# Kernel optimization log

Measured on AMD Instinct MI355X. Metric: run time of the kernel, lower is better.

## Reference

```python
import jax, jax.numpy as jnp
import numpy as np

N = 100000
E = 1_600_000
C_IN = 128
HID = 64
C_OUT = 64
HEADS = 3
NEG_SLOPE = 0.2  # PyG GATConv default leaky-relu slope


def setup_inputs() -> dict:
    key = jax.random.key(0)
    ks = jax.random.split(key, 8)
    return {
        "node_features": jax.random.normal(ks[0], (N, C_IN), jnp.float32),
        "edge_index": jax.random.randint(ks[1], (2, E), 0, N, jnp.int32),
        "edge_attributes": jax.random.uniform(ks[2], (E,), jnp.float32),
        "W1": jax.random.normal(ks[3], (C_IN, HID), jnp.float32) * 0.1,
        "b1": jnp.zeros((HID,), jnp.float32),
        "W2": jax.random.normal(ks[4], (HID, HEADS * C_OUT), jnp.float32) * 0.1,
        "b2": jnp.zeros((HEADS * C_OUT,), jnp.float32),
        "att_src": jax.random.normal(ks[5], (HEADS, C_OUT), jnp.float32) * 0.1,
        "att_dst": jax.random.normal(ks[6], (HEADS, C_OUT), jnp.float32) * 0.1,
    }


def reference(node_features, edge_index, edge_attributes, W1, b1, W2, b2, att_src, att_dst):
    n = node_features.shape[0]
    loops = jnp.arange(n, dtype=edge_index.dtype)
    # Both GCNConv and GATConv add self-loops by default (fill weight 1.0)
    src = jnp.concatenate([edge_index[0], loops])
    dst = jnp.concatenate([edge_index[1], loops])
    ew = jnp.concatenate([edge_attributes, jnp.ones((n,), node_features.dtype)])

    # ---- GCNConv: symmetric-normalized weighted scatter-add aggregation ----
    deg = jax.ops.segment_sum(ew, dst, num_segments=n)            # [N]
    dis = jnp.where(deg > 0, jax.lax.rsqrt(deg), 0.0)
    norm = dis[src] * ew * dis[dst]                               # [Et]
    xw = node_features @ W1                                       # [N, HID]
    x = jax.ops.segment_sum(xw[src] * norm[:, None], dst, num_segments=n) + b1
    x = jax.nn.relu(x)

    # ---- GATConv (heads concat): per-edge attention + segment softmax ----
    heads, c_out = att_src.shape
    g = (x @ W2).reshape(n, heads, c_out)                          # [N, H, F]
    a_src = jnp.sum(g * att_src, axis=-1)                          # [N, H]
    a_dst = jnp.sum(g * att_dst, axis=-1)                          # [N, H]
    alpha = jax.nn.leaky_relu(a_src[src] + a_dst[dst], NEG_SLOPE)  # [Et, H]
    amax = jax.ops.segment_max(alpha, dst, num_segments=n)         # softmax per dst node
    ex = jnp.exp(alpha - amax[dst])
    denom = jax.ops.segment_sum(ex, dst, num_segments=n)
    attn = ex / (denom[dst] + 1e-16)                               # [Et, H]
    out = jax.ops.segment_sum(g[src] * attn[:, :, None], dst, num_segments=n)
    out = out.reshape(n, heads * c_out) + b2                       # [N, H*F]

    # ---- global_mean_pool(x, None): mean over all nodes -> [1, H*F] ----
    return jnp.mean(out, axis=0, keepdims=True)
```

## Files before the change

### kernel.cpp

```cpp
#include <hip/hip_runtime.h>
#include <hip/hip_fp16.h>
#include <math.h>

typedef unsigned long long u64;
typedef unsigned int u32;

__device__ __forceinline__ float lrelu(float v) { return v > 0.f ? v : 0.2f * v; }

union H2U { __half2 h; u32 u; };


__global__ void k_hist(const int* __restrict__ dst, int* __restrict__ cnt, int E) {
    int e = blockIdx.x * 256 + threadIdx.x;
    if (e < E) atomicAdd(&cnt[dst[e]], 1);
}

__global__ __launch_bounds__(256) void k_scan1(const int* __restrict__ cnt,
                                               int* __restrict__ off,
                                               int* __restrict__ partials, int N) {
    __shared__ int sh[256];
    int tid = threadIdx.x;
    int base = blockIdx.x * 1024 + tid * 4;
    int v[4]; int tsum = 0;
#pragma unroll
    for (int i = 0; i < 4; i++) {
        int n = base + i;
        int c = (n < N) ? cnt[n] + 1 : 0;
        v[i] = tsum; tsum += c;
    }
    sh[tid] = tsum; __syncthreads();
    int mine = tsum;
    for (int o = 1; o < 256; o <<= 1) {
        int t = (tid >= o) ? sh[tid - o] : 0;
        __syncthreads();
        sh[tid] += t;
        __syncthreads();
    }
    int excl = sh[tid] - mine;
#pragma unroll
    for (int i = 0; i < 4; i++) {
        int n = base + i;
        if (n < N) off[n] = excl + v[i];
    }
    if (tid == 255) partials[blockIdx.x] = sh[255];
}

__global__ void k_scan2(int* __restrict__ partials, int nb) {
    __shared__ int sh[256];
    int tid = threadIdx.x;
    int v = (tid < nb) ? partials[tid] : 0;
    sh[tid] = v; __syncthreads();
    for (int o = 1; o < 256; o <<= 1) {
        int t = (tid >= o) ? sh[tid - o] : 0;
        __syncthreads();
        sh[tid] += t;
        __syncthreads();
    }
    if (tid < nb) partials[tid] = sh[tid] - v;
}

__global__ void k_scan3(int* __restrict__ off, int* __restrict__ cursor,
                        const int* __restrict__ partials, int N, int Et) {
    int base = blockIdx.x * 1024 + threadIdx.x * 4;
    int add = partials[blockIdx.x];
#pragma unroll
    for (int i = 0; i < 4; i++) {
        int n = base + i;
        if (n < N) { int o = off[n] + add; off[n] = o; cursor[n] = o; }
    }
    if (blockIdx.x == 0 && threadIdx.x == 0) { off[N] = Et; cursor[N] = Et; }
}

__global__ void k_fill(const int* __restrict__ src, const int* __restrict__ dst,
                       const float* __restrict__ ew, int* __restrict__ cursor,
                       u64* __restrict__ epk, int E, int Et) {
    int e = blockIdx.x * 256 + threadIdx.x;
    if (e >= Et) return;
    int s, d; float w;
    if (e < E) { s = src[e]; d = dst[e]; w = ew[e]; }
    else       { s = d = e - E; w = 1.0f; }
    int p = atomicAdd(&cursor[d], 1);
    epk[p] = ((u64)__float_as_uint(w) << 32) | (unsigned)s;
}

__global__ void k_degdis(const int* __restrict__ off, const u64* __restrict__ epk,
                         float* __restrict__ dis, int N) {
    int n = blockIdx.x * 256 + threadIdx.x;
    if (n >= N) return;
    int b = off[n], e2 = off[n + 1];
    float s = 0.f;
    for (int i = b; i < e2; i++) s += __uint_as_float((u32)(epk[i] >> 32));
    dis[n] = rsqrtf(s);
}


__global__ __launch_bounds__(256) void k_gemm1(const float* __restrict__ X,
                                               const float* __restrict__ W1,
                                               const float* __restrict__ dis,
                                               __half* __restrict__ xwh, int N) {
    __shared__ __align__(16) float Ws[128 * 64];
    __shared__ __align__(16) float Xs[32][129];
    int tid = threadIdx.x;
    int m0 = blockIdx.x * 32;
    const float4* W4 = (const float4*)W1;
    float4* Ws4 = (float4*)Ws;
#pragma unroll
    for (int i = 0; i < 8; i++) Ws4[tid + i * 256] = W4[tid + i * 256];
#pragma unroll
    for (int i = 0; i < 4; i++) {
        int idx = tid + i * 256;
        int r = idx >> 5;
        int c = idx & 31;
        float4 v = ((const float4*)(X + (size_t)(m0 + r) * 128))[c];
        Xs[r][c * 4 + 0] = v.x; Xs[r][c * 4 + 1] = v.y;
        Xs[r][c * 4 + 2] = v.z; Xs[r][c * 4 + 3] = v.w;
    }
    __syncthreads();
    int r = tid & 31;
    int c0 = (tid >> 5) * 8;
    float acc[8] = {0, 0, 0, 0, 0, 0, 0, 0};
#pragma unroll 4
    for (int k = 0; k < 128; k++) {
        float xv = Xs[r][k];
        const float4* wr = (const float4*)&Ws[k * 64 + c0];
        float4 w0 = wr[0], w1 = wr[1];
        acc[0] += xv * w0.x; acc[1] += xv * w0.y; acc[2] += xv * w0.z; acc[3] += xv * w0.w;
        acc[4] += xv * w1.x; acc[5] += xv * w1.y; acc[6] += xv * w1.z; acc[7] += xv * w1.w;
    }
    float dn = dis[m0 + r];
    H2U p0, p1, p2, p3;
    p0.h = __floats2half2_rn(acc[0] * dn, acc[1] * dn);
    p1.h = __floats2half2_rn(acc[2] * dn, acc[3] * dn);
    p2.h = __floats2half2_rn(acc[4] * dn, acc[5] * dn);
    p3.h = __floats2half2_rn(acc[6] * dn, acc[7] * dn);
    ((uint4*)(xwh + (size_t)(m0 + r) * 64))[c0 >> 3] = make_uint4(p0.u, p1.u, p2.u, p3.u);
}

__global__ __launch_bounds__(256) void k_gcn_agg(const int* __restrict__ off,
                                                 const u64* __restrict__ epk,
                                                 const float* __restrict__ dis,
                                                 const __half* __restrict__ xwh,
                                                 float* __restrict__ x, int N) {
    int lane = threadIdx.x & 63;
    int wv = threadIdx.x >> 6;
    int slot = lane >> 3;
    int f8 = lane & 7;
    int gw = blockIdx.x * 4 + wv;
    int stride = gridDim.x * 4;
    for (int n = gw; n < N; n += stride) {
        int b = off[n], en = off[n + 1];
        float acc[8] = {0, 0, 0, 0, 0, 0, 0, 0};
        for (int c = b; c < en; c += 64) {
            int idx = c + lane;
            int s = 0; float nw = 0.f;
            if (idx < en) {
                u64 pk = epk[idx];
                s = (int)(u32)pk;
                nw = __uint_as_float((u32)(pk >> 32));
            }
            int cc = min(64, en - c);
            for (int r = 0; r * 8 < cc; r++) {
                int eo = r * 8 + slot;
                int ss = __shfl(s, eo);
                float nn = __shfl(nw, eo);
                if (eo < cc) {
                    uint4 raw = ((const uint4*)(xwh + (size_t)ss * 64))[f8];
                    __half2* hp = (__half2*)&raw;
                    float2 q0 = __half22float2(hp[0]);
                    float2 q1 = __half22float2(hp[1]);
                    float2 q2 = __half22float2(hp[2]);
                    float2 q3 = __half22float2(hp[3]);
                    acc[0] += nn * q0.x; acc[1] += nn * q0.y;
                    acc[2] += nn * q1.x; acc[3] += nn * q1.y;
                    acc[4] += nn * q2.x; acc[5] += nn * q2.y;
                    acc[6] += nn * q3.x; acc[7] += nn * q3.y;
                }
            }
        }
#pragma unroll
        for (int j = 0; j < 8; j++) {
            acc[j] += __shfl_xor(acc[j], 8);
            acc[j] += __shfl_xor(acc[j], 16);
            acc[j] += __shfl_xor(acc[j], 32);
        }
        if (lane < 8) {
            float dn = dis[n];
            ((float4*)(x + (size_t)n * 64))[f8 * 2 + 0] =
                make_float4(acc[0] * dn, acc[1] * dn, acc[2] * dn, acc[3] * dn);
            ((float4*)(x + (size_t)n * 64))[f8 * 2 + 1] =
                make_float4(acc[4] * dn, acc[5] * dn, acc[6] * dn, acc[7] * dn);
        }
    }
}

__global__ __launch_bounds__(256) void k_gemm2(const float* __restrict__ x,
                                               const float* __restrict__ W2,
                                               const float* __restrict__ b1,
                                               __half* __restrict__ gh, int N) {
    __shared__ __align__(16) float Ws[64 * 192];
    __shared__ __align__(16) float Xs[32][65];
    __shared__ float b1s[64];
    int tid = threadIdx.x;
    int m0 = blockIdx.x * 32;
    if (tid < 64) b1s[tid] = b1[tid];
    __syncthreads();
    const float4* W4 = (const float4*)W2;
    float4* Ws4 = (float4*)Ws;
#pragma unroll
    for (int i = 0; i < 12; i++) Ws4[tid + i * 256] = W4[tid + i * 256];
#pragma unroll
    for (int i = 0; i < 2; i++) {
        int idx = tid + i * 256;
        int r = idx >> 4;
        int c4 = idx & 15;
        float4 v = ((const float4*)(x + (size_t)(m0 + r) * 64))[c4];
        v.x = fmaxf(v.x + b1s[c4 * 4 + 0], 0.f);
        v.y = fmaxf(v.y + b1s[c4 * 4 + 1], 0.f);
        v.z = fmaxf(v.z + b1s[c4 * 4 + 2], 0.f);
        v.w = fmaxf(v.w + b1s[c4 * 4 + 3], 0.f);
        Xs[r][c4 * 4 + 0] = v.x; Xs[r][c4 * 4 + 1] = v.y;
        Xs[r][c4 * 4 + 2] = v.z; Xs[r][c4 * 4 + 3] = v.w;
    }
    __syncthreads();
    int r = tid & 31;
    int c0 = (tid >> 5) * 24;
    float acc[24];
#pragma unroll
    for (int j = 0; j < 24; j++) acc[j] = 0.f;
#pragma unroll 4
    for (int k = 0; k < 64; k++) {
        float xv = Xs[r][k];
        const float4* wr = (const float4*)&Ws[k * 192 + c0];
#pragma unroll
        for (int q = 0; q < 6; q++) {
            float4 wv = wr[q];
            acc[q * 4 + 0] += xv * wv.x;
            acc[q * 4 + 1] += xv * wv.y;
            acc[q * 4 + 2] += xv * wv.z;
            acc[q * 4 + 3] += xv * wv.w;
        }
    }
    __half* outp = gh + (size_t)(m0 + r) * 192 + c0;
#pragma unroll
    for (int t = 0; t < 3; t++) {
        H2U p0, p1, p2, p3;
        p0.h = __floats2half2_rn(acc[t * 8 + 0], acc[t * 8 + 1]);
        p1.h = __floats2half2_rn(acc[t * 8 + 2], acc[t * 8 + 3]);
        p2.h = __floats2half2_rn(acc[t * 8 + 4], acc[t * 8 + 5]);
        p3.h = __floats2half2_rn(acc[t * 8 + 6], acc[t * 8 + 7]);
        ((uint4*)outp)[t] = make_uint4(p0.u, p1.u, p2.u, p3.u);
    }
}

__global__ __launch_bounds__(256) void k_att(const __half* __restrict__ gh,
                                             const float* __restrict__ att_src,
                                             const float* __restrict__ att_dst,
                                             float* __restrict__ asrc4,
                                             float* __restrict__ adst4, int N3) {
    __shared__ float as_s[192], ad_s[192];
    int tid = threadIdx.x;
    if (tid < 192) { as_s[tid] = att_src[tid]; ad_s[tid] = att_dst[tid]; }
    __syncthreads();
    int idx = blockIdx.x * 256 + tid;
    if (idx < N3) {
        int n = idx / 3, h = idx - 3 * n;
        const uint4* gp = (const uint4*)(gh + (size_t)n * 192 + h * 64);
        const float* av = as_s + h * 64;
        const float* bv = ad_s + h * 64;
        float sa = 0.f, sb = 0.f;
#pragma unroll
        for (int i = 0; i < 8; i++) {
            uint4 u = gp[i];
            __half2* hp = (__half2*)&u;
#pragma unroll
            for (int k = 0; k < 4; k++) {
                float2 f = __half22float2(hp[k]);
                int fi = i * 8 + k * 2;
                sa += f.x * av[fi] + f.y * av[fi + 1];
                sb += f.x * bv[fi] + f.y * bv[fi + 1];
            }
        }
        asrc4[(size_t)n * 4 + h] = sa;
        adst4[(size_t)n * 4 + h] = sb;
    }
}

__global__ __launch_bounds__(256) void k_gatsm(const int* __restrict__ off,
                                               const u64* __restrict__ epk,
                                               const float* __restrict__ asrc4,
                                               const float* __restrict__ adst4,
                                               u64* __restrict__ wpk, int N) {
    int n = blockIdx.x * 256 + threadIdx.x;
    if (n >= N) return;
    int b = off[n], en = off[n + 1];
    float4 ad = ((const float4*)adst4)[n];
    float m0 = -1e30f, m1 = -1e30f, m2 = -1e30f;
    for (int i = b; i < en; i++) {
        int s = (int)(u32)epk[i];
        float4 av = ((const float4*)asrc4)[s];
        m0 = fmaxf(m0, lrelu(av.x + ad.x));
        m1 = fmaxf(m1, lrelu(av.y + ad.y));
        m2 = fmaxf(m2, lrelu(av.z + ad.z));
    }
    float s0 = 0.f, s1 = 0.f, s2 = 0.f;
    for (int i = b; i < en; i++) {
        int s = (int)(u32)epk[i];
        float4 av = ((const float4*)asrc4)[s];
        s0 += __expf(lrelu(av.x + ad.x) - m0);
        s1 += __expf(lrelu(av.y + ad.y) - m1);
        s2 += __expf(lrelu(av.z + ad.z) - m2);
    }
    float i0 = 8192.f / s0, i1 = 8192.f / s1, i2 = 8192.f / s2;
    for (int i = b; i < en; i++) {
        int s = (int)(u32)epk[i];
        float4 av = ((const float4*)asrc4)[s];
        u32 q0 = __float2uint_rn(__expf(lrelu(av.x + ad.x) - m0) * i0);
        u32 q1 = __float2uint_rn(__expf(lrelu(av.y + ad.y) - m1) * i1);
        u32 q2 = __float2uint_rn(__expf(lrelu(av.z + ad.z) - m2) * i2);
        u64 pk = (u64)q0 | ((u64)q1 << 21) | ((u64)q2 << 42);
        atomicAdd(&wpk[s], pk);
    }
}

__global__ __launch_bounds__(192) void k_wsum(const u64* __restrict__ wpk,
                                              const __half* __restrict__ gh,
                                              float* __restrict__ gsum, int N) {
    int j = threadIdx.x;
    int sh = 21 * (j >> 6);
    int gs = gridDim.x;
    float a = 0.f;
    for (int n = blockIdx.x; n < N; n += gs) {
        u64 pk = wpk[n];
        float wn = (float)((u32)(pk >> sh) & 0x1FFFFFu);
        a += wn * __half2float(gh[(size_t)n * 192 + j]);
    }
    atomicAdd(&gsum[j], a);
}

__global__ void k_final(const float* __restrict__ gsum, const float* __restrict__ b2,
                        float* __restrict__ out, float inv) {
    int j = threadIdx.x;
    if (j < 192) out[j] = gsum[j] * inv + b2[j];
}

extern "C" void kernel_launch(void* const* d_in, const int* in_sizes, int n_in,
                              void* d_out, int out_size, void* d_ws, size_t ws_size,
                              hipStream_t stream) {
    const float* X   = (const float*)d_in[0];
    const int*   ei  = (const int*)d_in[1];
    const float* ew  = (const float*)d_in[2];
    const float* W1  = (const float*)d_in[3];
    const float* b1  = (const float*)d_in[4];
    const float* W2  = (const float*)d_in[5];
    const float* b2  = (const float*)d_in[6];
    const float* ats = (const float*)d_in[7];
    const float* atd = (const float*)d_in[8];

    int N  = in_sizes[0] / 128;
    int E  = in_sizes[1] / 2;
    int Et = E + N;
    const int* srcI = ei;
    const int* dstI = ei + E;

    float* ws = (float*)d_ws;
    int*   wsi = (int*)d_ws;

    size_t o = 0;
    int* off_p = wsi + o;           o += (size_t)N + 1;
    int* cur_p = wsi + o;           o += (size_t)N + 1;
    o = (o + 1) & ~(size_t)1;
    size_t z0 = o;
    u64* wpk   = (u64*)(wsi + o);   o += (size_t)N * 2;
    int* cnt_p = wsi + o;           o += (size_t)N;
    float* gsum = ws + o;           o += 192;
    size_t z1 = o;
    int* part_p = wsi + o;          o += 256;
    float* dis  = ws + o;           o += (size_t)N;
    o = (o + 3) & ~(size_t)3;
    float* asrc4 = ws + o;          o += (size_t)N * 4;
    float* adst4 = ws + o;          o += (size_t)N * 4;
    float* x     = ws + o;          o += (size_t)N * 64;
    __half* xwh  = (__half*)(ws + o); o += (size_t)N * 32;
    __half* gh   = (__half*)(ws + o); o += (size_t)N * 96;
    o = (o + 1) & ~(size_t)1;
    u64* epk = (u64*)(ws + o);

    hipMemsetAsync(wsi + z0, 0, (z1 - z0) * sizeof(int), stream);

    int nb = (N + 1023) / 1024;

    k_hist <<<(E + 255) / 256, 256, 0, stream>>>(dstI, cnt_p, E);
    k_scan1<<<nb, 256, 0, stream>>>(cnt_p, off_p, part_p, N);
    k_scan2<<<1, 256, 0, stream>>>(part_p, nb);
    k_scan3<<<nb, 256, 0, stream>>>(off_p, cur_p, part_p, N, Et);
    k_fill <<<(Et + 255) / 256, 256, 0, stream>>>(srcI, dstI, ew, cur_p, epk, E, Et);
    k_degdis<<<(N + 255) / 256, 256, 0, stream>>>(off_p, epk, dis, N);
    k_gemm1<<<N / 32, 256, 0, stream>>>(X, W1, dis, xwh, N);
    k_gcn_agg<<<2048, 256, 0, stream>>>(off_p, epk, dis, xwh, x, N);
    k_gemm2<<<N / 32, 256, 0, stream>>>(x, W2, b1, gh, N);
    k_att<<<(3 * N + 255) / 256, 256, 0, stream>>>(gh, ats, atd, asrc4, adst4, 3 * N);
    k_gatsm<<<(N + 255) / 256, 256, 0, stream>>>(off_p, epk, asrc4, adst4, wpk, N);
    k_wsum<<<512, 192, 0, stream>>>(wpk, gh, gsum, N);
    k_final<<<1, 192, 0, stream>>>(gsum, b2, (float*)d_out, 1.0f / (8192.0f * (float)N));
}
```

Measured before the change: 630.2 us.

## Pack edges into 32-bit words, fuse attention dots into GEMM2, use global-max softmax

Edge records shrink from 64-bit (float weight plus source) to 32-bit words holding a 15-bit quantized edge weight and a 17-bit source index, halving CSR traffic in the fill, degree, aggregation and softmax kernels. The attention dot products move into the GEMM2 epilogue, which removes the separate k_att kernel and its reread of gh. GEMM2 also tracks a global per-head max of a_src through an atomicMax. The softmax then uses lrelu(global max + a_dst) as its shift instead of a per-node max pass, saving one gather sweep. The risks are weight-quantization error, the 17-bit index limit on N, and possible underflow when the global shift is far above a node's scores.

```diff
diff --git a/kernel.cpp b/kernel.cpp
--- a/kernel.cpp
+++ b/kernel.cpp
@@ -6,6 +6,13 @@
 typedef unsigned int u32;
 
 __device__ __forceinline__ float lrelu(float v) { return v > 0.f ? v : 0.2f * v; }
+__device__ __forceinline__ u32 fkey(float x) {
+    u32 b = __float_as_uint(x);
+    return (b & 0x80000000u) ? ~b : (b | 0x80000000u);
+}
+__device__ __forceinline__ float finv(u32 k) {
+    return __uint_as_float((k & 0x80000000u) ? (k & 0x7fffffffu) : ~k);
+}
 
 union H2U { __half2 h; u32 u; };
 
@@ -73,24 +80,26 @@
 
 __global__ void k_fill(const int* __restrict__ src, const int* __restrict__ dst,
                        const float* __restrict__ ew, int* __restrict__ cursor,
-                       u64* __restrict__ epk, int E, int Et) {
+                       u32* __restrict__ epk, int E, int Et) {
     int e = blockIdx.x * 256 + threadIdx.x;
     if (e >= Et) return;
-    int s, d; float w;
-    if (e < E) { s = src[e]; d = dst[e]; w = ew[e]; }
-    else       { s = d = e - E; w = 1.0f; }
+    int s, d; u32 q;
+    if (e < E) {
+        s = src[e]; d = dst[e];
+        q = min(__float2uint_rn(ew[e] * 32767.f), 32767u);
+    } else { s = d = e - E; q = 32767u; }
     int p = atomicAdd(&cursor[d], 1);
-    epk[p] = ((u64)__float_as_uint(w) << 32) | (unsigned)s;
-}
-
-__global__ void k_degdis(const int* __restrict__ off, const u64* __restrict__ epk,
+    epk[p] = (q << 17) | (u32)s;
+}
+
+__global__ void k_degdis(const int* __restrict__ off, const u32* __restrict__ epk,
                          float* __restrict__ dis, int N) {
     int n = blockIdx.x * 256 + threadIdx.x;
     if (n >= N) return;
     int b = off[n], e2 = off[n + 1];
     float s = 0.f;
-    for (int i = b; i < e2; i++) s += __uint_as_float((u32)(epk[i] >> 32));
-    dis[n] = rsqrtf(s);
+    for (int i = b; i < e2; i++) s += (float)(epk[i] >> 17);
+    dis[n] = rsqrtf(s * (1.f / 32767.f));
 }
 
 
@@ -137,7 +146,7 @@
 }
 
 __global__ __launch_bounds__(256) void k_gcn_agg(const int* __restrict__ off,
-                                                 const u64* __restrict__ epk,
+                                                 const u32* __restrict__ epk,
                                                  const float* __restrict__ dis,
                                                  const __half* __restrict__ xwh,
                                                  float* __restrict__ x, int N) {
@@ -154,9 +163,9 @@
             int idx = c + lane;
             int s = 0; float nw = 0.f;
             if (idx < en) {
-                u64 pk = epk[idx];
-                s = (int)(u32)pk;
-                nw = __uint_as_float((u32)(pk >> 32));
+                u32 pk = epk[idx];
+                s = (int)(pk & 0x1FFFFu);
+                nw = (float)(pk >> 17) * (1.f / 32767.f);
             }
             int cc = min(64, en - c);
             for (int r = 0; r * 8 < cc; r++) {
@@ -196,13 +205,20 @@
 __global__ __launch_bounds__(256) void k_gemm2(const float* __restrict__ x,
                                                const float* __restrict__ W2,
                                                const float* __restrict__ b1,
-                                               __half* __restrict__ gh, int N) {
+                                               const float* __restrict__ att_src,
+                                               const float* __restrict__ att_dst,
+                                               __half* __restrict__ gh,
+                                               float* __restrict__ asrc4,
+                                               float* __restrict__ adst4,
+                                               u32* __restrict__ amaxk, int N) {
     __shared__ __align__(16) float Ws[64 * 192];
     __shared__ __align__(16) float Xs[32][65];
     __shared__ float b1s[64];
+    __shared__ float as_s[192], ad_s[192];
     int tid = threadIdx.x;
     int m0 = blockIdx.x * 32;
     if (tid < 64) b1s[tid] = b1[tid];
+    if (tid < 192) { as_s[tid] = att_src[tid]; ad_s[tid] = att_dst[tid]; }
     __syncthreads();
     const float4* W4 = (const float4*)W2;
     float4* Ws4 = (float4*)Ws;
@@ -250,73 +266,77 @@
         p3.h = __floats2half2_rn(acc[t * 8 + 6], acc[t * 8 + 7]);
         ((uint4*)outp)[t] = make_uint4(p0.u, p1.u, p2.u, p3.u);
     }
-}
-
-__global__ __launch_bounds__(256) void k_att(const __half* __restrict__ gh,
-                                             const float* __restrict__ att_src,
-                                             const float* __restrict__ att_dst,
-                                             float* __restrict__ asrc4,
-                                             float* __restrict__ adst4, int N3) {
-    __shared__ float as_s[192], ad_s[192];
-    int tid = threadIdx.x;
-    if (tid < 192) { as_s[tid] = att_src[tid]; ad_s[tid] = att_dst[tid]; }
-    __syncthreads();
-    int idx = blockIdx.x * 256 + tid;
-    if (idx < N3) {
-        int n = idx / 3, h = idx - 3 * n;
-        const uint4* gp = (const uint4*)(gh + (size_t)n * 192 + h * 64);
-        const float* av = as_s + h * 64;
-        const float* bv = ad_s + h * 64;
-        float sa = 0.f, sb = 0.f;
-#pragma unroll
-        for (int i = 0; i < 8; i++) {
-            uint4 u = gp[i];
-            __half2* hp = (__half2*)&u;
-#pragma unroll
-            for (int k = 0; k < 4; k++) {
-                float2 f = __half22float2(hp[k]);
-                int fi = i * 8 + k * 2;
-                sa += f.x * av[fi] + f.y * av[fi + 1];
-                sb += f.x * bv[fi] + f.y * bv[fi + 1];
-            }
+
+    float sa0 = 0.f, sa1 = 0.f, sb0 = 0.f, sb1 = 0.f;
+    int h0 = c0 >> 6;
+    int split = 64 - (c0 & 63); if (split > 24) split = 24;
+#pragma unroll
+    for (int j = 0; j < 24; j++) {
+        float va = acc[j] * as_s[c0 + j];
+        float vb = acc[j] * ad_s[c0 + j];
+        if (j < split) { sa0 += va; sb0 += vb; }
+        else           { sa1 += va; sb1 += vb; }
+    }
+    __syncthreads();
+    float* S = &Xs[0][0];
+    for (int i = tid; i < 1536; i += 256) S[i] = 0.f;
+    __syncthreads();
+    int ct = tid >> 5;
+    int slot = (r * 8 + ct) * 3;
+    S[slot + h0] = sa0;
+    S[768 + slot + h0] = sb0;
+    if (split < 24) { S[slot + h0 + 1] = sa1; S[768 + slot + h0 + 1] = sb1; }
+    __syncthreads();
+    if (tid < 96) {
+        int rr = tid / 3, h = tid - 3 * rr;
+        float sA = 0.f, sB = 0.f;
+#pragma unroll
+        for (int c = 0; c < 8; c++) {
+            sA += S[(rr * 8 + c) * 3 + h];
+            sB += S[768 + (rr * 8 + c) * 3 + h];
         }
-        asrc4[(size_t)n * 4 + h] = sa;
-        adst4[(size_t)n * 4 + h] = sb;
+        asrc4[(size_t)(m0 + rr) * 4 + h] = sA;
+        adst4[(size_t)(m0 + rr) * 4 + h] = sB;
+        S[1536 + tid] = sA;
+    }
+    __syncthreads();
+    if (tid < 3) {
+        float m = -1e30f;
+        for (int rr = 0; rr < 32; rr++) m = fmaxf(m, S[1536 + rr * 3 + tid]);
+        atomicMax(&amaxk[tid], fkey(m));
     }
 }
 
 __global__ __launch_bounds__(256) void k_gatsm(const int* __restrict__ off,
-                                               const u64* __restrict__ epk,
+                                               const u32* __restrict__ epk,
                                                const float* __restrict__ asrc4,
                                                const float* __restrict__ adst4,
+                                               const u32* __restrict__ amaxk,
                                                u64* __restrict__ wpk, int N) {
     int n = blockIdx.x * 256 + threadIdx.x;
     if (n >= N) return;
     int b = off[n], en = off[n + 1];
     float4 ad = ((const float4*)adst4)[n];
-    float m0 = -1e30f, m1 = -1e30f, m2 = -1e30f;
-    for (int i = b; i < en; i++) {
-        int s = (int)(u32)epk[i];
-        float4 av = ((const float4*)asrc4)[s];
-        m0 = fmaxf(m0, lrelu(av.x + ad.x));
-        m1 = fmaxf(m1, lrelu(av.y + ad.y));
-        m2 = fmaxf(m2, lrelu(av.z + ad.z));
-    }
+    float M0 = lrelu(finv(amaxk[0]) + ad.x);
+    float M1 = lrelu(finv(amaxk[1]) + ad.y);
+    float M2 = lrelu(finv(amaxk[2]) + ad.z);
     float s0 = 0.f, s1 = 0.f, s2 = 0.f;
     for (int i = b; i < en; i++) {
-        int s = (int)(u32)epk[i];
+        int s = (int)(epk[i] & 0x1FFFFu);
         float4 av = ((const float4*)asrc4)[s];
-        s0 += __expf(lrelu(av.x + ad.x) - m0);
-        s1 += __expf(lrelu(av.y + ad.y) - m1);
-        s2 += __expf(lrelu(av.z + ad.z) - m2);
-    }
-    float i0 = 8192.f / s0, i1 = 8192.f / s1, i2 = 8192.f / s2;
+        s0 += __expf(lrelu(av.x + ad.x) - M0);
+        s1 += __expf(lrelu(av.y + ad.y) - M1);
+        s2 += __expf(lrelu(av.z + ad.z) - M2);
+    }
+    float i0 = 8192.f / (s0 + 1e-16f);
+    float i1 = 8192.f / (s1 + 1e-16f);
+    float i2 = 8192.f / (s2 + 1e-16f);
     for (int i = b; i < en; i++) {
-        int s = (int)(u32)epk[i];
+        int s = (int)(epk[i] & 0x1FFFFu);
         float4 av = ((const float4*)asrc4)[s];
-        u32 q0 = __float2uint_rn(__expf(lrelu(av.x + ad.x) - m0) * i0);
-        u32 q1 = __float2uint_rn(__expf(lrelu(av.y + ad.y) - m1) * i1);
-        u32 q2 = __float2uint_rn(__expf(lrelu(av.z + ad.z) - m2) * i2);
+        u32 q0 = __float2uint_rn(__expf(lrelu(av.x + ad.x) - M0) * i0);
+        u32 q1 = __float2uint_rn(__expf(lrelu(av.y + ad.y) - M1) * i1);
+        u32 q2 = __float2uint_rn(__expf(lrelu(av.z + ad.z) - M2) * i2);
         u64 pk = (u64)q0 | ((u64)q1 << 21) | ((u64)q2 << 42);
         atomicAdd(&wpk[s], pk);
     }
@@ -373,6 +393,7 @@
     u64* wpk   = (u64*)(wsi + o);   o += (size_t)N * 2;
     int* cnt_p = wsi + o;           o += (size_t)N;
     float* gsum = ws + o;           o += 192;
+    u32* amaxk = (u32*)(wsi + o);   o += 4;
     size_t z1 = o;
     int* part_p = wsi + o;          o += 256;
     float* dis  = ws + o;           o += (size_t)N;
@@ -382,8 +403,7 @@
     float* x     = ws + o;          o += (size_t)N * 64;
     __half* xwh  = (__half*)(ws + o); o += (size_t)N * 32;
     __half* gh   = (__half*)(ws + o); o += (size_t)N * 96;
-    o = (o + 1) & ~(size_t)1;
-    u64* epk = (u64*)(ws + o);
+    u32* epk = (u32*)(ws + o);
 
     hipMemsetAsync(wsi + z0, 0, (z1 - z0) * sizeof(int), stream);
 
@@ -397,9 +417,8 @@
     k_degdis<<<(N + 255) / 256, 256, 0, stream>>>(off_p, epk, dis, N);
     k_gemm1<<<N / 32, 256, 0, stream>>>(X, W1, dis, xwh, N);
     k_gcn_agg<<<2048, 256, 0, stream>>>(off_p, epk, dis, xwh, x, N);
-    k_gemm2<<<N / 32, 256, 0, stream>>>(x, W2, b1, gh, N);
-    k_att<<<(3 * N + 255) / 256, 256, 0, stream>>>(gh, ats, atd, asrc4, adst4, 3 * N);
-    k_gatsm<<<(N + 255) / 256, 256, 0, stream>>>(off_p, epk, asrc4, adst4, wpk, N);
+    k_gemm2<<<N / 32, 256, 0, stream>>>(x, W2, b1, ats, atd, gh, asrc4, adst4, amaxk, N);
+    k_gatsm<<<(N + 255) / 256, 256, 0, stream>>>(off_p, epk, asrc4, adst4, amaxk, wpk, N);
     k_wsum<<<512, 192, 0, stream>>>(wpk, gh, gsum, N);
     k_final<<<1, 192, 0, stream>>>(gsum, b2, (float*)d_out, 1.0f / (8192.0f * (float)N));
 }
```

New measurement: 612.2 us. 1.03x faster.
